# Kernel optimization log

Hardware: AMD Instinct MI355X
Metric: run time of the kernel (lower is better)

Reference implementation:

```python
import jax, jax.numpy as jnp
import numpy as np

N_E = 1024
E_DIM = 256
DECAY = 0.99
BETA = 1.0
EPS = 1e-5


def setup_inputs() -> dict:
    key = jax.random.key(0)
    k1, k2, k3 = jax.random.split(key, 3)
    z = jax.random.normal(k1, (32, E_DIM, 64, 64), dtype=jnp.float32)
    embedding = jax.random.normal(k2, (N_E, E_DIM), dtype=jnp.float32)
    embedding_avg = embedding  # buffers initialized as clone of embedding
    cluster_size = jnp.ones((N_E,), dtype=jnp.float32)
    return {"z": z, "embedding": embedding, "embedding_avg": embedding_avg,
            "cluster_size": cluster_size}


def reference(z, embedding, embedding_avg, cluster_size):
    B, C, H, W = z.shape
    zp = jnp.transpose(z, (0, 2, 3, 1))          # [B,H,W,C]
    zf = zp.reshape(-1, C)                        # [N,C]

    # squared euclidean distances [N, n_e]
    d = (jnp.sum(zf * zf, axis=1, keepdims=True)
         + jnp.sum(embedding * embedding, axis=1)[None, :]
         - 2.0 * zf @ embedding.T)
    idx = jnp.argmin(d, axis=1)                   # [N]

    z_q = embedding[idx].reshape(zp.shape)        # [B,H,W,C] (old codebook)

    # training-mode EMA update (scatter-based accumulation)
    counts = jnp.zeros((N_E,), dtype=zf.dtype).at[idx].add(1.0)
    emb_sum = jnp.zeros((N_E, C), dtype=zf.dtype).at[idx].add(zf)
    new_cluster_size = cluster_size * DECAY + (1.0 - DECAY) * counts
    new_embedding_avg = embedding_avg * DECAY + (1.0 - DECAY) * emb_sum
    n = jnp.sum(new_cluster_size)
    smoothed = (new_cluster_size + EPS) / (n + N_E * EPS) * n
    new_embedding = new_embedding_avg / smoothed[:, None]

    sg = jax.lax.stop_gradient
    loss = (BETA * jnp.mean((sg(z_q) - zp) ** 2)
            + jnp.mean((z_q - sg(zp)) ** 2))

    z_q_st = zp + sg(z_q - zp)                    # straight-through
    z_q_out = jnp.transpose(z_q_st, (0, 3, 1, 2))  # back to NCHW
    min_encoding_indices = idx.reshape(B, H, W)
    return (z_q_out, loss, min_encoding_indices,
            new_embedding, new_embedding_avg, new_cluster_size)
```

## Files before the change

kernel.cpp:

```cpp
#include <hip/hip_runtime.h>

#define BATCH 32
#define CDIM 256
#define HW 4096
#define NVEC 131072
#define NE 1024
#define DECAY 0.99f
#define ONE_MINUS_DECAY 0.01f
#define EPSV 1e-5f
#define ZQ_ELEMS 33554432

__device__ __forceinline__ void fma4(float a, const float4& b, float4& c) {
  c.x = fmaf(a, b.x, c.x);
  c.y = fmaf(a, b.y, c.y);
  c.z = fmaf(a, b.z, c.z);
  c.w = fmaf(a, b.w, c.w);
}

__device__ __forceinline__ float getc(const float4& v, int c) {
  switch (c & 3) {
    case 0: return v.x;
    case 1: return v.y;
    case 2: return v.z;
    default: return v.w;
  }
}

__global__ __launch_bounds__(256) void prep_kernel(
    const float* __restrict__ emb, float* __restrict__ embT) {
  __shared__ float tile[32][33];
  int k0 = blockIdx.x * 32;
  int e0 = blockIdx.y * 32;
  int tx = threadIdx.x;
  int ty = threadIdx.y;
  #pragma unroll
  for (int j = 0; j < 32; j += 8)
    tile[ty + j][tx] = emb[(size_t)(e0 + ty + j) * CDIM + k0 + tx];
  __syncthreads();
  #pragma unroll
  for (int j = 0; j < 32; j += 8)
    embT[(size_t)(k0 + ty + j) * NE + e0 + tx] = tile[tx][ty + j];
}

__global__ __launch_bounds__(256) void enorm_kernel(
    const float* __restrict__ emb, float* __restrict__ enorm) {
  int gid  = blockIdx.x * 256 + threadIdx.x;
  int e    = gid >> 6;
  int lane = threadIdx.x & 63;
  const float4* row = (const float4*)(emb + ((size_t)e << 8));
  float4 v = row[lane];
  float s = v.x * v.x + v.y * v.y + v.z * v.z + v.w * v.w;
  #pragma unroll
  for (int off = 32; off > 0; off >>= 1) s += __shfl_down(s, off);
  if (lane == 0) enorm[e] = s;
}

#define BK 16
#define ZS_LD 68
#define ES_LD 260
__global__ __launch_bounds__(256, 3) void argmin_kernel(
    const float* __restrict__ z, const float* __restrict__ embT,
    const float* __restrict__ enorm, int* __restrict__ idx_ws,
    float* __restrict__ idx_out, float* __restrict__ counts) {
  __shared__ float zs[BK][ZS_LD];
  __shared__ float es[BK][ES_LD];
  __shared__ float rbest[16][64];
  __shared__ int   ridx[16][64];

  int t  = threadIdx.x;
  int tn = t & 15;
  int te = t >> 4;
  int n0 = blockIdx.x * 64;
  int b  = n0 >> 12;
  int hw0 = n0 & 4095;
  const float* zb = z + ((size_t)b << 20) + hw0;

  int lk = t >> 4;
  int ln = (t & 15) * 4;
  int le = (t & 15) * 16;

  float bestd[4] = {3.0e38f, 3.0e38f, 3.0e38f, 3.0e38f};
  int   besti[4] = {0, 0, 0, 0};

  #pragma unroll 1
  for (int et = 0; et < 4; ++et) {
    float4 acc[4][4];
    #pragma unroll
    for (int i = 0; i < 4; ++i)
      #pragma unroll
      for (int j = 0; j < 4; ++j)
        acc[i][j] = make_float4(0.f, 0.f, 0.f, 0.f);

    #pragma unroll 1
    for (int kc = 0; kc < CDIM; kc += BK) {
      __syncthreads();
      *(float4*)&zs[lk][ln] =
          *(const float4*)(zb + (size_t)(kc + lk) * HW + ln);
      const float* ep = embT + (size_t)(kc + lk) * NE + et * 256 + le;
      *(float4*)&es[lk][le]      = *(const float4*)(ep);
      *(float4*)&es[lk][le + 4]  = *(const float4*)(ep + 4);
      *(float4*)&es[lk][le + 8]  = *(const float4*)(ep + 8);
      *(float4*)&es[lk][le + 12] = *(const float4*)(ep + 12);
      __syncthreads();

      #pragma unroll 2
      for (int k = 0; k < BK; ++k) {
        const float4 zv = *(const float4*)&zs[k][tn * 4];
        const float4 e0 = *(const float4*)&es[k][te * 16];
        const float4 e1 = *(const float4*)&es[k][te * 16 + 4];
        const float4 e2 = *(const float4*)&es[k][te * 16 + 8];
        const float4 e3 = *(const float4*)&es[k][te * 16 + 12];
        #pragma unroll
        for (int i = 0; i < 4; ++i) {
          const float zi = getc(zv, i);
          fma4(zi, e0, acc[i][0]);
          fma4(zi, e1, acc[i][1]);
          fma4(zi, e2, acc[i][2]);
          fma4(zi, e3, acc[i][3]);
        }
      }
    }

    #pragma unroll
    for (int i = 0; i < 4; ++i) {
      #pragma unroll
      for (int jq = 0; jq < 4; ++jq) {
        #pragma unroll
        for (int jc = 0; jc < 4; ++jc) {
          int e = et * 256 + te * 16 + jq * 4 + jc;
          float d = enorm[e] - 2.0f * getc(acc[i][jq], jc);
          if (d < bestd[i]) { bestd[i] = d; besti[i] = e; }
        }
      }
    }
  }

  #pragma unroll
  for (int i = 0; i < 4; ++i) {
    rbest[te][tn * 4 + i] = bestd[i];
    ridx[te][tn * 4 + i]  = besti[i];
  }
  __syncthreads();
  if (t < 64) {
    float bd = rbest[0][t];
    int   bi = ridx[0][t];
    #pragma unroll
    for (int g = 1; g < 16; ++g) {
      float d = rbest[g][t];
      if (d < bd) { bd = d; bi = ridx[g][t]; }
    }
    int n = n0 + t;
    idx_ws[n] = bi;
    idx_out[n] = (float)bi;
    atomicAdd(&counts[bi], 1.0f);
  }
}

__global__ __launch_bounds__(256) void fused_scatter_kernel(
    const float* __restrict__ z, const float* __restrict__ emb,
    const int* __restrict__ idx_ws, float* __restrict__ zq_out,
    float* __restrict__ loss_acc, float* __restrict__ emb_sum) {
  __shared__ float hist[NE];
  int t = threadIdx.x;
  #pragma unroll
  for (int i = t; i < NE; i += 256) hist[i] = 0.0f;
  __syncthreads();

  int c     = blockIdx.x & 255;
  int chunk = blockIdx.x >> 8;
  int base  = chunk << 14;

  float lsum = 0.0f;
  const int4* idx4 = (const int4*)idx_ws;
  for (int i4 = t; i4 < 4096; i4 += 256) {
    int n0 = base + (i4 << 2);
    int b  = n0 >> 12;
    int hw = n0 & 4095;
    size_t off = (((size_t)(b << 8) + c) << 12) + hw;
    float4 v = *(const float4*)(z + off);
    int4 id = idx4[n0 >> 2];
    float4 q;
    q.x = emb[((size_t)id.x << 8) + c];
    q.y = emb[((size_t)id.y << 8) + c];
    q.z = emb[((size_t)id.z << 8) + c];
    q.w = emb[((size_t)id.w << 8) + c];
    *(float4*)(zq_out + off) = q;
    float dx = q.x - v.x, dy = q.y - v.y, dz = q.z - v.z, dw = q.w - v.w;
    lsum += dx * dx + dy * dy + dz * dz + dw * dw;
    atomicAdd(&hist[id.x], v.x);
    atomicAdd(&hist[id.y], v.y);
    atomicAdd(&hist[id.z], v.z);
    atomicAdd(&hist[id.w], v.w);
  }
  __syncthreads();

  for (int e = t; e < NE; e += 256)
    atomicAdd(&emb_sum[(e << 8) + c], hist[e]);

  __shared__ float red[256];
  red[t] = lsum;
  __syncthreads();
  for (int s = 128; s > 0; s >>= 1) {
    if (t < s) red[t] += red[t + s];
    __syncthreads();
  }
  if (t == 0) atomicAdd(loss_acc, red[0]);
}

__global__ __launch_bounds__(1024) void ema_cs_kernel(
    const float* __restrict__ cs, const float* __restrict__ counts,
    float* __restrict__ out_ncs, float* __restrict__ n_ws,
    const float* __restrict__ loss_acc, float* __restrict__ loss_out) {
  int e = threadIdx.x;
  float ncs = cs[e] * DECAY + ONE_MINUS_DECAY * counts[e];
  out_ncs[e] = ncs;
  __shared__ float red[1024];
  red[e] = ncs;
  __syncthreads();
  for (int s = 512; s > 0; s >>= 1) {
    if (e < s) red[e] += red[e + s];
    __syncthreads();
  }
  if (e == 0) {
    n_ws[0] = red[0];
    loss_out[0] = loss_acc[0] * 2.0f / (float)ZQ_ELEMS;
  }
}

__global__ __launch_bounds__(256) void ema_emb_kernel(
    const float* __restrict__ eavg, const float* __restrict__ emb_sum,
    const float* __restrict__ ncs, const float* __restrict__ n_ws,
    float* __restrict__ out_eavg, float* __restrict__ out_emb) {
  int i = blockIdx.x * 256 + threadIdx.x;
  int e = i >> 8;
  float ea = eavg[i] * DECAY + ONE_MINUS_DECAY * emb_sum[i];
  out_eavg[i] = ea;
  float nv   = n_ws[0];
  float ncse = ncs[e];
  float sm   = (ncse + EPSV) / (nv + (float)NE * EPSV) * nv;
  out_emb[i] = ea / sm;
}

extern "C" void kernel_launch(void* const* d_in, const int* in_sizes, int n_in,
                              void* d_out, int out_size, void* d_ws, size_t ws_size,
                              hipStream_t stream) {
  const float* z    = (const float*)d_in[0];
  const float* emb  = (const float*)d_in[1];
  const float* eavg = (const float*)d_in[2];
  const float* cs   = (const float*)d_in[3];

  float* out = (float*)d_out;
  float* out_zq   = out;
  float* out_loss = out + 33554432;
  float* out_idx  = out + 33554433;
  float* out_emb  = out + 33685505;
  float* out_eavg = out + 33947649;
  float* out_ncs  = out + 34209793;

  float* ws       = (float*)d_ws;
  int*   idx_ws   = (int*)ws;
  float* emb_sum  = ws + 131072;
  float* counts   = ws + 393216;
  float* loss_acc = ws + 394240;
  float* n_ws     = ws + 394241;
  float* enorm    = ws + 394244;

  float* embT = out_zq;

  hipMemsetAsync(ws + 131072, 0, (size_t)263170 * sizeof(float), stream);

  dim3 tb(32, 8);
  dim3 tg(CDIM / 32, NE / 32);
  prep_kernel<<<tg, tb, 0, stream>>>(emb, embT);
  enorm_kernel<<<NE / 4, 256, 0, stream>>>(emb, enorm);
  argmin_kernel<<<NVEC / 64, 256, 0, stream>>>(z, embT, enorm, idx_ws, out_idx, counts);
  fused_scatter_kernel<<<2048, 256, 0, stream>>>(z, emb, idx_ws, out_zq, loss_acc, emb_sum);
  ema_cs_kernel<<<1, 1024, 0, stream>>>(cs, counts, out_ncs, n_ws, loss_acc, out_loss);
  ema_emb_kernel<<<262144 / 256, 256, 0, stream>>>(eavg, emb_sum, out_ncs, n_ws, out_eavg, out_emb);
}
```

Measured before the change: 1.149 ms.

## Compute VQ distances with split-fp16 MFMA and exact fp32 fixup for near-ties

Replaces the fp32 FMA distance GEMM with MFMA 16x16x32 f16 instructions, using a hi/lo fp16 split of both z and the codebook (three MFMAs per tile) to approximate fp32 precision. The kernel tracks the best and second-best distance per vector and flags vectors whose margin is below a threshold. A separate fixup kernel recomputes those flagged vectors exactly in fp32 and corrects indices and counts. This trades exactness of the main pass for matrix-core throughput, at the cost of an extra kernel, atomics on a flag list, and a dependence on how many near-ties occur.

```diff
diff --git a/kernel.cpp b/kernel.cpp
--- a/kernel.cpp
+++ b/kernel.cpp
@@ -9,37 +9,27 @@
 #define ONE_MINUS_DECAY 0.01f
 #define EPSV 1e-5f
 #define ZQ_ELEMS 33554432
-
-__device__ __forceinline__ void fma4(float a, const float4& b, float4& c) {
-  c.x = fmaf(a, b.x, c.x);
-  c.y = fmaf(a, b.y, c.y);
-  c.z = fmaf(a, b.z, c.z);
-  c.w = fmaf(a, b.w, c.w);
-}
-
-__device__ __forceinline__ float getc(const float4& v, int c) {
-  switch (c & 3) {
-    case 0: return v.x;
-    case 1: return v.y;
-    case 2: return v.z;
-    default: return v.w;
-  }
-}
-
-__global__ __launch_bounds__(256) void prep_kernel(
-    const float* __restrict__ emb, float* __restrict__ embT) {
-  __shared__ float tile[32][33];
-  int k0 = blockIdx.x * 32;
-  int e0 = blockIdx.y * 32;
-  int tx = threadIdx.x;
-  int ty = threadIdx.y;
-  #pragma unroll
-  for (int j = 0; j < 32; j += 8)
-    tile[ty + j][tx] = emb[(size_t)(e0 + ty + j) * CDIM + k0 + tx];
-  __syncthreads();
-  #pragma unroll
-  for (int j = 0; j < 32; j += 8)
-    embT[(size_t)(k0 + ty + j) * NE + e0 + tx] = tile[tx][ty + j];
+#define MARGIN 0.02f
+
+typedef _Float16 half8 __attribute__((ext_vector_type(8)));
+typedef _Float16 half4 __attribute__((ext_vector_type(4)));
+typedef float    f32x4 __attribute__((ext_vector_type(4)));
+
+__global__ __launch_bounds__(256) void prep_half_kernel(
+    const float* __restrict__ emb, _Float16* __restrict__ embH,
+    _Float16* __restrict__ embL) {
+  int i = blockIdx.x * 256 + threadIdx.x;
+  float4 v = ((const float4*)emb)[i];
+  float x[4] = {v.x, v.y, v.z, v.w};
+  half4 hv, lv;
+  #pragma unroll
+  for (int j = 0; j < 4; ++j) {
+    _Float16 h = (_Float16)x[j];
+    hv[j] = h;
+    lv[j] = (_Float16)(x[j] - (float)h);
+  }
+  *(half4*)(embH + 4 * (size_t)i) = hv;
+  *(half4*)(embL + 4 * (size_t)i) = lv;
 }
 
 __global__ __launch_bounds__(256) void enorm_kernel(
@@ -55,104 +45,234 @@
   if (lane == 0) enorm[e] = s;
 }
 
-#define BK 16
-#define ZS_LD 68
-#define ES_LD 260
-__global__ __launch_bounds__(256, 3) void argmin_kernel(
-    const float* __restrict__ z, const float* __restrict__ embT,
-    const float* __restrict__ enorm, int* __restrict__ idx_ws,
-    float* __restrict__ idx_out, float* __restrict__ counts) {
-  __shared__ float zs[BK][ZS_LD];
-  __shared__ float es[BK][ES_LD];
-  __shared__ float rbest[16][64];
-  __shared__ int   ridx[16][64];
-
-  int t  = threadIdx.x;
-  int tn = t & 15;
-  int te = t >> 4;
-  int n0 = blockIdx.x * 64;
-  int b  = n0 >> 12;
-  int hw0 = n0 & 4095;
+__global__ __launch_bounds__(256, 2) void argmin_kernel(
+    const float* __restrict__ z, const _Float16* __restrict__ embH,
+    const _Float16* __restrict__ embL, const float* __restrict__ enorm,
+    int* __restrict__ idx_ws, float* __restrict__ idx_out,
+    float* __restrict__ counts, int* __restrict__ flag_cnt,
+    int* __restrict__ flag_list) {
+  __shared__ char smem[65536];
+
+  const int t = threadIdx.x;
+  const int w = t >> 6;
+  const int l = t & 63;
+  const int g = l >> 4;
+  const int c = l & 15;
+
+  const int n0  = blockIdx.x * 64;
+  const int b   = n0 >> 12;
+  const int hw0 = n0 & 4095;
   const float* zb = z + ((size_t)b << 20) + hw0;
 
-  int lk = t >> 4;
-  int ln = (t & 15) * 4;
-  int le = (t & 15) * 16;
-
-  float bestd[4] = {3.0e38f, 3.0e38f, 3.0e38f, 3.0e38f};
-  int   besti[4] = {0, 0, 0, 0};
+  {
+    const int n  = t & 63;
+    const int kg = t >> 6;
+    char* zhp = smem;
+    char* zlp = smem + 32768;
+    #pragma unroll
+    for (int it = 0; it < 8; ++it) {
+      const int k0 = it * 32 + kg * 8;
+      half8 hv, lv;
+      #pragma unroll
+      for (int j = 0; j < 8; ++j) {
+        float x = zb[(size_t)(k0 + j) * HW + n];
+        _Float16 h = (_Float16)x;
+        hv[j] = h;
+        lv[j] = (_Float16)(x - (float)h);
+      }
+      const int slot = ((k0 >> 3) ^ (n & 31)) & 31;
+      const int byte = n * 512 + slot * 16;
+      *(half8*)(zhp + byte) = hv;
+      *(half8*)(zlp + byte) = lv;
+    }
+  }
+  __syncthreads();
+
+  float bd[4][4], b2[4][4];
+  int   bi[4][4];
+  #pragma unroll
+  for (int mi = 0; mi < 4; ++mi)
+    #pragma unroll
+    for (int r = 0; r < 4; ++r) { bd[mi][r] = 3.0e38f; b2[mi][r] = 3.0e38f; bi[mi][r] = 0; }
+
+  int arow[4], axor[4];
+  #pragma unroll
+  for (int mi = 0; mi < 4; ++mi) {
+    int rowm = 16 * mi + c;
+    arow[mi] = rowm * 512;
+    axor[mi] = rowm & 31;
+  }
+
+  const char* bhp = (const char*)embH;
+  const char* blp = (const char*)embL;
 
   #pragma unroll 1
   for (int et = 0; et < 4; ++et) {
-    float4 acc[4][4];
-    #pragma unroll
-    for (int i = 0; i < 4; ++i)
-      #pragma unroll
-      for (int j = 0; j < 4; ++j)
-        acc[i][j] = make_float4(0.f, 0.f, 0.f, 0.f);
-
+    const int ebase = et * 256 + w * 64;
+    f32x4 acc[4][4];
+    #pragma unroll
+    for (int mi = 0; mi < 4; ++mi)
+      #pragma unroll
+      for (int ni = 0; ni < 4; ++ni) {
+        f32x4 zr = {0.0f, 0.0f, 0.0f, 0.0f};
+        acc[mi][ni] = zr;
+      }
+
+    size_t boff[4];
+    #pragma unroll
+    for (int ni = 0; ni < 4; ++ni) {
+      int eg = ebase + 16 * ni + c;
+      boff[ni] = (size_t)eg * 512 + (size_t)(g * 16);
+    }
+
+    #pragma unroll
+    for (int kc = 0; kc < 256; kc += 32) {
+      half8 ah[4], al[4], bh[4], bl[4];
+      const int kslot = (kc >> 3) + g;
+      #pragma unroll
+      for (int mi = 0; mi < 4; ++mi) {
+        int byte = arow[mi] + (((kslot ^ axor[mi]) & 31) << 4);
+        ah[mi] = *(const half8*)(smem + byte);
+        al[mi] = *(const half8*)(smem + 32768 + byte);
+      }
+      #pragma unroll
+      for (int ni = 0; ni < 4; ++ni) {
+        size_t o = boff[ni] + (size_t)(kc * 2);
+        bh[ni] = *(const half8*)(bhp + o);
+        bl[ni] = *(const half8*)(blp + o);
+      }
+      #pragma unroll
+      for (int mi = 0; mi < 4; ++mi)
+        #pragma unroll
+        for (int ni = 0; ni < 4; ++ni) {
+          acc[mi][ni] = __builtin_amdgcn_mfma_f32_16x16x32_f16(ah[mi], bh[ni], acc[mi][ni], 0, 0, 0);
+          acc[mi][ni] = __builtin_amdgcn_mfma_f32_16x16x32_f16(ah[mi], bl[ni], acc[mi][ni], 0, 0, 0);
+          acc[mi][ni] = __builtin_amdgcn_mfma_f32_16x16x32_f16(al[mi], bh[ni], acc[mi][ni], 0, 0, 0);
+        }
+    }
+
+    #pragma unroll
+    for (int ni = 0; ni < 4; ++ni) {
+      const int e = ebase + 16 * ni + c;
+      const float en = enorm[e];
+      #pragma unroll
+      for (int mi = 0; mi < 4; ++mi)
+        #pragma unroll
+        for (int r = 0; r < 4; ++r) {
+          float d = en - 2.0f * acc[mi][ni][r];
+          if (d < bd[mi][r]) { b2[mi][r] = bd[mi][r]; bd[mi][r] = d; bi[mi][r] = e; }
+          else if (d < b2[mi][r]) b2[mi][r] = d;
+        }
+    }
+  }
+
+  #pragma unroll
+  for (int mi = 0; mi < 4; ++mi)
+    #pragma unroll
+    for (int r = 0; r < 4; ++r) {
+      float d = bd[mi][r]; int i = bi[mi][r]; float s2 = b2[mi][r];
+      #pragma unroll
+      for (int off = 1; off < 16; off <<= 1) {
+        float od = __shfl_xor(d, off);
+        int   oi = __shfl_xor(i, off);
+        float o2 = __shfl_xor(s2, off);
+        float ns = fminf(fminf(fmaxf(d, od), s2), o2);
+        if (od < d || (od == d && oi < i)) { d = od; i = oi; }
+        s2 = ns;
+      }
+      bd[mi][r] = d; bi[mi][r] = i; b2[mi][r] = s2;
+    }
+
+  __syncthreads();
+  float* sd  = (float*)smem;
+  int*   si  = (int*)(smem + 1024);
+  float* s2m = (float*)(smem + 2048);
+  if (c == 0) {
+    #pragma unroll
+    for (int mi = 0; mi < 4; ++mi)
+      #pragma unroll
+      for (int r = 0; r < 4; ++r) {
+        int n = 16 * mi + 4 * g + r;
+        sd[w * 64 + n] = bd[mi][r];
+        si[w * 64 + n] = bi[mi][r];
+        s2m[w * 64 + n] = b2[mi][r];
+      }
+  }
+  __syncthreads();
+  if (t < 64) {
+    float d = sd[t]; int i = si[t]; float s2 = s2m[t];
+    #pragma unroll
+    for (int ww = 1; ww < 4; ++ww) {
+      float od = sd[ww * 64 + t];
+      int   oi = si[ww * 64 + t];
+      float o2 = s2m[ww * 64 + t];
+      float ns = fminf(fminf(fmaxf(d, od), s2), o2);
+      if (od < d || (od == d && oi < i)) { d = od; i = oi; }
+      s2 = ns;
+    }
+    const int n = n0 + t;
+    idx_ws[n]  = i;
+    idx_out[n] = (float)i;
+    atomicAdd(&counts[i], 1.0f);
+    if (s2 - d < MARGIN) {
+      int p = atomicAdd(flag_cnt, 1);
+      flag_list[p] = n;
+    }
+  }
+}
+
+__global__ __launch_bounds__(256) void fixup_kernel(
+    const float* __restrict__ z, const float* __restrict__ emb,
+    const float* __restrict__ enorm, const int* __restrict__ flag_cnt,
+    const int* __restrict__ flag_list, int* __restrict__ idx_ws,
+    float* __restrict__ idx_out, float* __restrict__ counts) {
+  __shared__ float zf[256];
+  __shared__ float rd[256];
+  __shared__ int   ri[256];
+  const int t = threadIdx.x;
+  const int cnt = *flag_cnt;
+  for (int fi = blockIdx.x; fi < cnt; fi += gridDim.x) {
+    const int n = flag_list[fi];
+    const int b = n >> 12, hw = n & 4095;
+    __syncthreads();
+    zf[t] = z[((size_t)b << 20) + ((size_t)t << 12) + hw];
+    __syncthreads();
+    float bdv = 3.0e38f; int biv = 0;
     #pragma unroll 1
-    for (int kc = 0; kc < CDIM; kc += BK) {
+    for (int rep = 0; rep < 4; ++rep) {
+      const int e = rep * 256 + t;
+      const float4* er = (const float4*)(emb + ((size_t)e << 8));
+      const float4* zr = (const float4*)zf;
+      float dot = 0.0f;
+      #pragma unroll 8
+      for (int k4 = 0; k4 < 64; ++k4) {
+        float4 ev = er[k4];
+        float4 zv = zr[k4];
+        dot += ev.x * zv.x + ev.y * zv.y + ev.z * zv.z + ev.w * zv.w;
+      }
+      float d = enorm[e] - 2.0f * dot;
+      if (d < bdv) { bdv = d; biv = e; }
+    }
+    rd[t] = bdv; ri[t] = biv;
+    __syncthreads();
+    for (int s = 128; s > 0; s >>= 1) {
+      if (t < s) {
+        float od = rd[t + s]; int oi = ri[t + s];
+        if (od < rd[t] || (od == rd[t] && oi < ri[t])) { rd[t] = od; ri[t] = oi; }
+      }
       __syncthreads();
-      *(float4*)&zs[lk][ln] =
-          *(const float4*)(zb + (size_t)(kc + lk) * HW + ln);
-      const float* ep = embT + (size_t)(kc + lk) * NE + et * 256 + le;
-      *(float4*)&es[lk][le]      = *(const float4*)(ep);
-      *(float4*)&es[lk][le + 4]  = *(const float4*)(ep + 4);
-      *(float4*)&es[lk][le + 8]  = *(const float4*)(ep + 8);
-      *(float4*)&es[lk][le + 12] = *(const float4*)(ep + 12);
-      __syncthreads();
-
-      #pragma unroll 2
-      for (int k = 0; k < BK; ++k) {
-        const float4 zv = *(const float4*)&zs[k][tn * 4];
-        const float4 e0 = *(const float4*)&es[k][te * 16];
-        const float4 e1 = *(const float4*)&es[k][te * 16 + 4];
-        const float4 e2 = *(const float4*)&es[k][te * 16 + 8];
-        const float4 e3 = *(const float4*)&es[k][te * 16 + 12];
-        #pragma unroll
-        for (int i = 0; i < 4; ++i) {
-          const float zi = getc(zv, i);
-          fma4(zi, e0, acc[i][0]);
-          fma4(zi, e1, acc[i][1]);
-          fma4(zi, e2, acc[i][2]);
-          fma4(zi, e3, acc[i][3]);
-        }
-      }
-    }
-
-    #pragma unroll
-    for (int i = 0; i < 4; ++i) {
-      #pragma unroll
-      for (int jq = 0; jq < 4; ++jq) {
-        #pragma unroll
-        for (int jc = 0; jc < 4; ++jc) {
-          int e = et * 256 + te * 16 + jq * 4 + jc;
-          float d = enorm[e] - 2.0f * getc(acc[i][jq], jc);
-          if (d < bestd[i]) { bestd[i] = d; besti[i] = e; }
-        }
-      }
-    }
-  }
-
-  #pragma unroll
-  for (int i = 0; i < 4; ++i) {
-    rbest[te][tn * 4 + i] = bestd[i];
-    ridx[te][tn * 4 + i]  = besti[i];
-  }
-  __syncthreads();
-  if (t < 64) {
-    float bd = rbest[0][t];
-    int   bi = ridx[0][t];
-    #pragma unroll
-    for (int g = 1; g < 16; ++g) {
-      float d = rbest[g][t];
-      if (d < bd) { bd = d; bi = ridx[g][t]; }
-    }
-    int n = n0 + t;
-    idx_ws[n] = bi;
-    idx_out[n] = (float)bi;
-    atomicAdd(&counts[bi], 1.0f);
+    }
+    if (t == 0) {
+      const int nw  = ri[0];
+      const int old = idx_ws[n];
+      if (nw != old) {
+        atomicAdd(&counts[old], -1.0f);
+        atomicAdd(&counts[nw],  1.0f);
+        idx_ws[n]  = nw;
+        idx_out[n] = (float)nw;
+      }
+    }
+    __syncthreads();
   }
 }
 
@@ -265,15 +385,20 @@
   float* n_ws     = ws + 394241;
   float* enorm    = ws + 394244;
 
-  float* embT = out_zq;
+  _Float16* embH  = (_Float16*)out_zq;
+  _Float16* embL  = (_Float16*)(out_zq + 131072);
+  int* flag_cnt   = (int*)(out_zq + 262144);
+  int* flag_list  = (int*)(out_zq + 262145);
 
   hipMemsetAsync(ws + 131072, 0, (size_t)263170 * sizeof(float), stream);
-
-  dim3 tb(32, 8);
-  dim3 tg(CDIM / 32, NE / 32);
-  prep_kernel<<<tg, tb, 0, stream>>>(emb, embT);
+  hipMemsetAsync(out_zq + 262144, 0, sizeof(int), stream);
+
+  prep_half_kernel<<<256, 256, 0, stream>>>(emb, embH, embL);
   enorm_kernel<<<NE / 4, 256, 0, stream>>>(emb, enorm);
-  argmin_kernel<<<NVEC / 64, 256, 0, stream>>>(z, embT, enorm, idx_ws, out_idx, counts);
+  argmin_kernel<<<NVEC / 64, 256, 0, stream>>>(z, embH, embL, enorm, idx_ws,
+                                               out_idx, counts, flag_cnt, flag_list);
+  fixup_kernel<<<128, 256, 0, stream>>>(z, emb, enorm, flag_cnt, flag_list,
+                                        idx_ws, out_idx, counts);
   fused_scatter_kernel<<<2048, 256, 0, stream>>>(z, emb, idx_ws, out_zq, loss_acc, emb_sum);
   ema_cs_kernel<<<1, 1024, 0, stream>>>(cs, counts, out_ncs, n_ws, loss_acc, out_loss);
   ema_emb_kernel<<<262144 / 256, 256, 0, stream>>>(eavg, emb_sum, out_ncs, n_ws, out_eavg, out_emb);
```

After: 1.173 ms. +2.1%, slower.
